# Optimization experiments

Measured on AMD Instinct MI355X. Metric: run time of the kernel, lower is better.

The kernel has to match this reference:

```python
import jax, jax.numpy as jnp
import numpy as np

NUM_HEADS = 16
EPS = 1e-5
CHUNK = 128  # chunk length for the chunked recurrent-state scan


def _linear_attention(x, Wq, Wk, Wv, Wo, bo):
    B, T, E = x.shape
    H = NUM_HEADS
    d = E // H

    def proj(W):
        # nn.Linear(bias=False): y = x @ W.T ; split heads -> (B,H,T,d)
        return (x @ W.T).reshape(B, T, H, d).transpose(0, 2, 1, 3)

    phi_q = jax.nn.elu(proj(Wq)) + 1.0
    phi_k = jax.nn.elu(proj(Wk)) + 1.0
    V = proj(Wv)

    nC = T // CHUNK
    # (nC, B, H, C, d) so lax.scan iterates over chunks of time
    def to_chunks(a):
        return a.reshape(B, H, nC, CHUNK, d).transpose(2, 0, 1, 3, 4)

    qc, kc, vc = to_chunks(phi_q), to_chunks(phi_k), to_chunks(V)
    mask = jnp.tril(jnp.ones((CHUNK, CHUNK), x.dtype))  # causal incl. diagonal

    S0 = jnp.zeros((B, H, d, d), x.dtype)  # running sum of k v^T
    z0 = jnp.zeros((B, H, d), x.dtype)     # running sum of phi_k

    def step(carry, inp):
        S, z = carry
        q, k, v = inp  # (B,H,C,d)
        A = jnp.einsum('bhid,bhjd->bhij', q, k) * mask
        num = jnp.einsum('bhij,bhjd->bhid', A, v) + jnp.einsum('bhid,bhde->bhie', q, S)
        den = jnp.sum(A, axis=-1) + jnp.einsum('bhid,bhd->bhi', q, z) + EPS
        out = num / den[..., None]
        S = S + jnp.einsum('bhjd,bhje->bhde', k, v)
        z = z + jnp.sum(k, axis=2)
        return (S, z), out

    _, outs = jax.lax.scan(step, (S0, z0), (qc, kc, vc))  # (nC,B,H,C,d)
    out = outs.transpose(1, 2, 0, 3, 4).reshape(B, H, T, d)
    out = out.transpose(0, 2, 1, 3).reshape(B, T, E)
    # out_proj (dropout p=0 / eval -> identity)
    return out @ Wo.T + bo


def setup_inputs() -> dict:
    key = jax.random.key(0)
    ks = jax.random.split(key, 6)
    B, T, E = 2, 2048, 1024
    s = 1.0 / np.sqrt(E)
    return {
        'x': jax.random.normal(ks[0], (B, T, E), jnp.float32),
        'Wq': jax.random.normal(ks[1], (E, E), jnp.float32) * s,
        'Wk': jax.random.normal(ks[2], (E, E), jnp.float32) * s,
        'Wv': jax.random.normal(ks[3], (E, E), jnp.float32) * s,
        'Wo': jax.random.normal(ks[4], (E, E), jnp.float32) * s,
        'bo': jnp.zeros((E,), jnp.float32),
    }


def reference(x, Wq, Wk, Wv, Wo, bo):
    return _linear_attention(x, Wq, Wk, Wv, Wo, bo)
```

## Files before the change

kernel.cpp:

```cpp
#include <hip/hip_runtime.h>
#include <hip/hip_bf16.h>
#include <stdint.h>

typedef __attribute__((ext_vector_type(4)))  float  floatx4;
typedef __attribute__((ext_vector_type(8)))  short  short8;
typedef __attribute__((ext_vector_type(8)))  unsigned short ushortx8;
typedef __attribute__((ext_vector_type(4)))  unsigned short ushortx4;

#define B_  2
#define T_  2048
#define E_  1024
#define H_  16
#define D_  64
#define C_  128
#define NC_ 16
#define M_  4096
#define EPS_ 1e-5f

__device__ __forceinline__ unsigned short f2b(float f) {
    union { float f; unsigned int u; } v; v.f = f;
    unsigned int r = v.u + 0x7fffu + ((v.u >> 16) & 1u);
    return (unsigned short)(r >> 16);
}
__device__ __forceinline__ float b2f(unsigned short b) {
    union { unsigned int u; float f; } v; v.u = ((unsigned int)b) << 16;
    return v.f;
}

__device__ __forceinline__ int stage_seg(int i) { return (i & 3) ^ ((i >> 3) & 3); }
__device__ __forceinline__ int frag_slot(int lane) {
    int m = lane & 15, q = lane >> 4;
    return m * 4 + (q ^ ((m >> 1) & 3));
}

__global__ __launch_bounds__(256) void convert_all(const float* __restrict__ x,
                                                   const float* __restrict__ Wq,
                                                   const float* __restrict__ Wk,
                                                   const float* __restrict__ Wv,
                                                   const float* __restrict__ Wo,
                                                   unsigned short* __restrict__ dst) {
    int i = (blockIdx.x * 256 + threadIdx.x) * 4;
    const float* s; int off;
    if (i < M_ * E_) { s = x; off = i; }
    else {
        int j = i - M_ * E_;
        int which = j >> 20;
        s = (which == 0) ? Wq : (which == 1) ? Wk : (which == 2) ? Wv : Wo;
        off = j & ((1 << 20) - 1);
    }
    float4 f = *(const float4*)(s + off);
    ushortx4 o;
    o[0] = f2b(f.x); o[1] = f2b(f.y); o[2] = f2b(f.z); o[3] = f2b(f.w);
    *(ushortx4*)(dst + i) = o;
}

__global__ __launch_bounds__(256) void gemm_qkv(const unsigned short* __restrict__ A,
                                                const unsigned short* __restrict__ Bm,
                                                unsigned short* __restrict__ Cb) {
    const int N = 3 * E_, K = E_;
    __shared__ __align__(16) unsigned short smem[32768];
    unsigned short* at0 = smem;
    unsigned short* bt0 = smem + 8192;
    unsigned short* at1 = smem + 16384;
    unsigned short* bt1 = smem + 24576;
    int tid = threadIdx.x;
    int wave = tid >> 6, lane = tid & 63;
    int wr = wave >> 1, wc = wave & 1;
    int m = lane & 15, q = lane >> 4;
    int srow = lane >> 2, sseg = stage_seg(lane);
    int fs = frag_slot(lane);
    int row0 = blockIdx.y * 128, col0 = blockIdx.x * 128;
    floatx4 acc[4][4];
    for (int i = 0; i < 4; i++) for (int j = 0; j < 4; j++) acc[i][j] = floatx4{0.f, 0.f, 0.f, 0.f};

    auto stageA = [&](unsigned short* at, int k0) {
        for (int p = 0; p < 4; p++) {
            int t = p * 4 + wave;
            const unsigned short* ga = A + (size_t)(row0 + (t & 7) * 16 + srow) * K + k0 + (t >> 3) * 32 + sseg * 8;
            __builtin_amdgcn_global_load_lds((const __attribute__((address_space(1))) unsigned int*)ga,
                (__attribute__((address_space(3))) unsigned int*)(at + t * 512), 16, 0, 0);
        }
    };
    auto stageB = [&](unsigned short* bt, int k0) {
        for (int p = 0; p < 4; p++) {
            int u = p * 4 + wave;
            const unsigned short* gb = Bm + (size_t)(col0 + (u & 7) * 16 + srow) * K + k0 + (u >> 3) * 32 + sseg * 8;
            __builtin_amdgcn_global_load_lds((const __attribute__((address_space(1))) unsigned int*)gb,
                (__attribute__((address_space(3))) unsigned int*)(bt + u * 512), 16, 0, 0);
        }
    };
    short8 af[4], bf[4];
    auto frags = [&](const unsigned short* at, const unsigned short* bt, int kh) {
        for (int mi = 0; mi < 4; mi++) af[mi] = *(const short8*)(at + (kh * 8 + wr * 4 + mi) * 512 + fs * 8);
        for (int ni = 0; ni < 4; ni++) bf[ni] = *(const short8*)(bt + (kh * 8 + wc * 4 + ni) * 512 + fs * 8);
    };
    auto mfma16 = [&]() {
        __builtin_amdgcn_s_setprio(1);
        for (int mi = 0; mi < 4; mi++)
            for (int ni = 0; ni < 4; ni++)
                acc[mi][ni] = __builtin_amdgcn_mfma_f32_16x16x32_bf16(af[mi], bf[ni], acc[mi][ni], 0, 0, 0);
        __builtin_amdgcn_s_setprio(0);
    };

    stageA(at0, 0); stageB(bt0, 0);
    for (int k0 = 0; k0 < K; k0 += 128) {
        stageA(at1, k0 + 64);
        asm volatile("s_waitcnt vmcnt(4)" ::: "memory");
        __builtin_amdgcn_s_barrier();
        frags(at0, bt0, 0);
        mfma16();
        frags(at0, bt0, 1);
        stageB(bt1, k0 + 64);
        mfma16();
        __builtin_amdgcn_s_barrier();
        if (k0 + 128 < K) {
            stageA(at0, k0 + 128);
            asm volatile("s_waitcnt vmcnt(4)" ::: "memory");
        } else {
            asm volatile("s_waitcnt vmcnt(0)" ::: "memory");
        }
        __builtin_amdgcn_s_barrier();
        frags(at1, bt1, 0);
        mfma16();
        frags(at1, bt1, 1);
        if (k0 + 128 < K) stageB(bt0, k0 + 128);
        mfma16();
        __builtin_amdgcn_s_barrier();
    }

    unsigned short* epi = smem + wave * 2176;
    bool isphi = (col0 < 2 * E_);
    for (int half = 0; half < 2; half++) {
        if (half) asm volatile("" ::: "memory");
        for (int mi2 = 0; mi2 < 2; mi2++) {
            int mi = half * 2 + mi2;
            for (int ni = 0; ni < 4; ni++)
                for (int reg = 0; reg < 4; reg++) {
                    int lr = mi2 * 16 + q * 4 + reg;
                    float v = acc[mi][ni][reg];
                    if (isphi) v = (v > 0.f) ? (v + 1.f) : __expf(v);
                    epi[lr * 68 + ni * 16 + m] = f2b(v);
                }
        }
        for (int i = 0; i < 4; i++) {
            int s = i * 64 + lane;
            int lr = s >> 3, seg = s & 7;
            const unsigned short* p = epi + lr * 68 + seg * 8;
            ushortx4 lo = *(const ushortx4*)(p);
            ushortx4 hi = *(const ushortx4*)(p + 4);
            ushortx8 val;
            for (int e = 0; e < 4; e++) { val[e] = lo[e]; val[e + 4] = hi[e]; }
            int row = row0 + wr * 64 + half * 32 + lr;
            int col = col0 + wc * 64 + seg * 8;
            *(ushortx8*)(Cb + (size_t)row * N + col) = val;
        }
    }
}

__global__ __launch_bounds__(256) void gemm_out(const unsigned short* __restrict__ A,
                                                const unsigned short* __restrict__ Bm,
                                                const float* __restrict__ bias,
                                                float* __restrict__ Cf) {
    const int N = E_, K = E_;
    __shared__ __align__(16) unsigned short smem[24576];
    unsigned short* at0 = smem;
    unsigned short* bt0 = smem + 8192;
    unsigned short* at1 = smem + 12288;
    unsigned short* bt1 = smem + 20480;
    int tid = threadIdx.x;
    int wave = tid >> 6, lane = tid & 63;
    int wr = wave >> 1, wc = wave & 1;
    int m = lane & 15, q = lane >> 4;
    int srow = lane >> 2, sseg = stage_seg(lane);
    int fs = frag_slot(lane);
    int row0 = blockIdx.y * 128, col0 = blockIdx.x * 64;
    floatx4 acc[4][2];
    for (int i = 0; i < 4; i++) for (int j = 0; j < 2; j++) acc[i][j] = floatx4{0.f, 0.f, 0.f, 0.f};

    auto stageA = [&](unsigned short* at, int k0) {
        for (int p = 0; p < 4; p++) {
            int t = p * 4 + wave;
            const unsigned short* ga = A + (size_t)(row0 + (t & 7) * 16 + srow) * K + k0 + (t >> 3) * 32 + sseg * 8;
            __builtin_amdgcn_global_load_lds((const __attribute__((address_space(1))) unsigned int*)ga,
                (__attribute__((address_space(3))) unsigned int*)(at + t * 512), 16, 0, 0);
        }
    };
    auto stageB = [&](unsigned short* bt, int k0) {
        for (int p = 0; p < 2; p++) {
            int u = p * 4 + wave;
            const unsigned short* gb = Bm + (size_t)(col0 + (u & 3) * 16 + srow) * K + k0 + (u >> 2) * 32 + sseg * 8;
            __builtin_amdgcn_global_load_lds((const __attribute__((address_space(1))) unsigned int*)gb,
                (__attribute__((address_space(3))) unsigned int*)(bt + u * 512), 16, 0, 0);
        }
    };
    short8 af[4], bf[2];
    auto frags = [&](const unsigned short* at, const unsigned short* bt, int kh) {
        for (int mi = 0; mi < 4; mi++) af[mi] = *(const short8*)(at + (kh * 8 + wr * 4 + mi) * 512 + fs * 8);
        for (int ci = 0; ci < 2; ci++) bf[ci] = *(const short8*)(bt + (kh * 4 + wc * 2 + ci) * 512 + fs * 8);
    };
    auto mfma8 = [&]() {
        __builtin_amdgcn_s_setprio(1);
        for (int mi = 0; mi < 4; mi++)
            for (int ci = 0; ci < 2; ci++)
                acc[mi][ci] = __builtin_amdgcn_mfma_f32_16x16x32_bf16(af[mi], bf[ci], acc[mi][ci], 0, 0, 0);
        __builtin_amdgcn_s_setprio(0);
    };

    stageA(at0, 0); stageB(bt0, 0);
    for (int k0 = 0; k0 < K; k0 += 128) {
        stageA(at1, k0 + 64);
        asm volatile("s_waitcnt vmcnt(4)" ::: "memory");
        __builtin_amdgcn_s_barrier();
        frags(at0, bt0, 0);
        mfma8();
        frags(at0, bt0, 1);
        stageB(bt1, k0 + 64);
        mfma8();
        __builtin_amdgcn_s_barrier();
        if (k0 + 128 < K) {
            stageA(at0, k0 + 128);
            asm volatile("s_waitcnt vmcnt(4)" ::: "memory");
        } else {
            asm volatile("s_waitcnt vmcnt(0)" ::: "memory");
        }
        __builtin_amdgcn_s_barrier();
        frags(at1, bt1, 0);
        mfma8();
        frags(at1, bt1, 1);
        if (k0 + 128 < K) stageB(bt0, k0 + 128);
        mfma8();
        __builtin_amdgcn_s_barrier();
    }

    int qrow = q * 4;
    for (int ci = 0; ci < 2; ci++) {
        int col = col0 + wc * 32 + ci * 16 + m;
        float bv = bias[col];
        for (int mi = 0; mi < 4; mi++)
            for (int r2 = 0; r2 < 4; r2++) {
                int row = row0 + wr * 64 + mi * 16 + qrow + r2;
                Cf[(size_t)row * N + col] = acc[mi][ci][r2] + bv;
            }
    }
}

__global__ __launch_bounds__(256) void chunk_sums(const unsigned short* __restrict__ qkv,
                                                  float* __restrict__ Sc, float* __restrict__ zc) {
    int c = blockIdx.x, h = blockIdx.y, bb = blockIdx.z;
    __shared__ __align__(16) unsigned short Kt[64 * 132];
    __shared__ __align__(16) unsigned short Vt[80 * 132];
    int tid = threadIdx.x;
    int lane = tid & 63, w = tid >> 6;
    size_t rowb = (size_t)bb * T_ + (size_t)c * C_;
    int kcol = E_ + h * D_, vcol = 2 * E_ + h * D_;

    {
        int r4 = (tid >> 3) * 4;
        int seg = (tid & 7) * 8;
        ushortx8 kv[4], vv[4];
        for (int t = 0; t < 4; t++) {
            size_t g = (rowb + r4 + t) * 3072;
            kv[t] = *(const ushortx8*)(qkv + g + kcol + seg);
            vv[t] = *(const ushortx8*)(qkv + g + vcol + seg);
        }
        for (int e = 0; e < 8; e++) {
            ushortx4 ka, va;
            for (int t = 0; t < 4; t++) { ka[t] = kv[t][e]; va[t] = vv[t][e]; }
            *(ushortx4*)(Kt + (seg + e) * 132 + r4) = ka;
            *(ushortx4*)(Vt + (seg + e) * 132 + r4) = va;
        }
    }
    if (tid < 128) Vt[64 * 132 + tid] = 0x3f80;
    __syncthreads();

    floatx4 acc[5];
    for (int ni = 0; ni < 5; ni++) acc[ni] = floatx4{0.f, 0.f, 0.f, 0.f};
    int lm = lane & 15, lk = (lane >> 4) * 8;
    for (int k0 = 0; k0 < 128; k0 += 32) {
        short8 af = *(const short8*)(Kt + (w * 16 + lm) * 132 + k0 + lk);
        for (int ni = 0; ni < 5; ni++) {
            short8 bf = *(const short8*)(Vt + (ni * 16 + lm) * 132 + k0 + lk);
            acc[ni] = __builtin_amdgcn_mfma_f32_16x16x32_bf16(af, bf, acc[ni], 0, 0, 0);
        }
    }
    size_t base = ((size_t)(bb * H_ + h) * NC_ + c) * (size_t)(D_ * D_);
    int r0 = w * 16 + (lane >> 4) * 4;
    for (int ni = 0; ni < 4; ni++)
        for (int reg = 0; reg < 4; reg++)
            Sc[base + (size_t)(r0 + reg) * D_ + ni * 16 + lm] = acc[ni][reg];
    if (lm == 0) {
        size_t zb = ((size_t)(bb * H_ + h) * NC_ + c) * D_;
        for (int reg = 0; reg < 4; reg++) zc[zb + r0 + reg] = acc[4][reg];
    }
}

__global__ __launch_bounds__(256) void prefix_state(const float* __restrict__ Sc,
                                                    const float* __restrict__ zc,
                                                    unsigned short* __restrict__ Spt,
                                                    float* __restrict__ zp) {
    int h = blockIdx.x, bb = blockIdx.y;
    int tid = threadIdx.x;
    size_t bh = (size_t)bb * H_ + h;
    const float* S = Sc + bh * NC_ * (size_t)(D_ * D_);
    unsigned short* P = Spt + bh * NC_ * (size_t)(D_ * D_);
    int p = tid * 16, r = p >> 6, c0 = p & 63;
    float a[16];
    for (int i = 0; i < 16; i++) a[i] = 0.f;
    for (int cc = 0; cc < NC_; cc++) {
        unsigned short* Pc = P + (size_t)cc * (D_ * D_);
        for (int i = 0; i < 16; i++)
            Pc[(c0 + i) * D_ + r] = f2b(a[i]);
        const float* Sj = S + (size_t)cc * (D_ * D_) + p;
        for (int q = 0; q < 16; q += 4) {
            float4 f = *(const float4*)(Sj + q);
            a[q] += f.x; a[q + 1] += f.y; a[q + 2] += f.z; a[q + 3] += f.w;
        }
    }
    if (tid < 64) {
        const float* z = zc + bh * NC_ * (size_t)D_;
        float* zo = zp + bh * NC_ * (size_t)D_;
        float za = 0.f;
        for (int cc = 0; cc < NC_; cc++) { zo[cc * D_ + tid] = za; za += z[cc * D_ + tid]; }
    }
}

__global__ __launch_bounds__(256) void attn_kernel(const unsigned short* __restrict__ qkv,
                                                   const unsigned short* __restrict__ Spt,
                                                   const float* __restrict__ zp,
                                                   unsigned short* __restrict__ attn) {
    int c = blockIdx.x, h = blockIdx.y, bb = blockIdx.z;
    __shared__ __align__(16) unsigned short ks[128 * 68];
    __shared__ __align__(16) unsigned short vt[64 * 132];
    __shared__ __align__(16) unsigned short ovl[128 * 36];
    int tid = threadIdx.x;
    int lane = tid & 63, w = tid >> 6;
    int lm = lane & 15, lq = lane >> 4;
    size_t rowb = (size_t)bb * T_ + (size_t)c * C_;
    int qcol = h * D_, kcol = E_ + h * D_, vcol = 2 * E_ + h * D_;
    size_t pbase = ((size_t)bb * H_ + h) * NC_ + c;

    for (int s = 0; s < 4; s++) {
        int off = s * 256 + tid;
        int r = off >> 3, seg = (off & 7) * 8;
        ushortx8 k8 = *(const ushortx8*)(qkv + (rowb + r) * 3072 + kcol + seg);
        *(ushortx8*)(ks + r * 68 + seg) = k8;
    }
    {
        int r4 = (tid >> 3) * 4;
        int seg = (tid & 7) * 8;
        ushortx8 vv[4];
        for (int t = 0; t < 4; t++)
            vv[t] = *(const ushortx8*)(qkv + (rowb + r4 + t) * 3072 + vcol + seg);
        for (int e = 0; e < 8; e++) {
            ushortx4 va;
            for (int t = 0; t < 4; t++) va[t] = vv[t][e];
            *(ushortx4*)(vt + (seg + e) * 132 + r4) = va;
        }
    }

    short8 aq[2][2];
    for (int mi = 0; mi < 2; mi++)
        for (int kk = 0; kk < 2; kk++)
            aq[mi][kk] = *(const short8*)(qkv + (rowb + w * 32 + mi * 16 + lm) * 3072 + qcol + kk * 32 + lq * 8);

    floatx4 acc[2][4];
    for (int mi = 0; mi < 2; mi++) for (int ni = 0; ni < 4; ni++) acc[mi][ni] = floatx4{0.f, 0.f, 0.f, 0.f};
    {
        const unsigned short* sp = Spt + pbase * (size_t)(D_ * D_);
        for (int kk = 0; kk < 2; kk++)
            for (int ni = 0; ni < 4; ni++) {
                short8 bs = *(const short8*)(sp + (ni * 16 + lm) * D_ + kk * 32 + lq * 8);
                for (int mi = 0; mi < 2; mi++)
                    acc[mi][ni] = __builtin_amdgcn_mfma_f32_16x16x32_bf16(aq[mi][kk], bs, acc[mi][ni], 0, 0, 0);
            }
    }
    float dsum[2][4];
    {
        float4 z4 = *(const float4*)(zp + pbase * D_ + lm * 4);
        for (int mi = 0; mi < 2; mi++)
            for (int reg = 0; reg < 4; reg++) {
                int row = w * 32 + mi * 16 + lq * 4 + reg;
                ushortx4 q4 = *(const ushortx4*)(qkv + (rowb + row) * 3072 + qcol + lm * 4);
                dsum[mi][reg] = b2f(q4[0]) * z4.x + b2f(q4[1]) * z4.y + b2f(q4[2]) * z4.z + b2f(q4[3]) * z4.w;
            }
    }
    __syncthreads();

    for (int jt = 0; jt <= w; jt++) {
        floatx4 pa[2][2];
        for (int mi = 0; mi < 2; mi++) for (int ct = 0; ct < 2; ct++) pa[mi][ct] = floatx4{0.f, 0.f, 0.f, 0.f};
        for (int kk = 0; kk < 2; kk++)
            for (int ct = 0; ct < 2; ct++) {
                short8 bk = *(const short8*)(ks + (jt * 32 + ct * 16 + lm) * 68 + kk * 32 + lq * 8);
                for (int mi = 0; mi < 2; mi++)
                    pa[mi][ct] = __builtin_amdgcn_mfma_f32_16x16x32_bf16(aq[mi][kk], bk, pa[mi][ct], 0, 0, 0);
            }
        bool diag = (jt == w);
        for (int mi = 0; mi < 2; mi++)
            for (int ct = 0; ct < 2; ct++)
                for (int reg = 0; reg < 4; reg++) {
                    int il = mi * 16 + lq * 4 + reg;
                    int jl = ct * 16 + lm;
                    float v = pa[mi][ct][reg];
                    if (diag && jl > il) v = 0.f;
                    dsum[mi][reg] += v;
                    ovl[(w * 32 + il) * 36 + jl] = f2b(v);
                }
        short8 ap[2];
        for (int mi = 0; mi < 2; mi++)
            ap[mi] = *(const short8*)(ovl + (w * 32 + mi * 16 + lm) * 36 + lq * 8);
        for (int ni = 0; ni < 4; ni++) {
            short8 bv = *(const short8*)(vt + (ni * 16 + lm) * 132 + jt * 32 + lq * 8);
            for (int mi = 0; mi < 2; mi++)
                acc[mi][ni] = __builtin_amdgcn_mfma_f32_16x16x32_bf16(ap[mi], bv, acc[mi][ni], 0, 0, 0);
        }
    }

    for (int off = 1; off < 16; off <<= 1)
        for (int mi = 0; mi < 2; mi++)
            for (int reg = 0; reg < 4; reg++)
                dsum[mi][reg] += __shfl_xor(dsum[mi][reg], off);

    for (int mi = 0; mi < 2; mi++)
        for (int reg = 0; reg < 4; reg++) {
            float inv = 1.f / (dsum[mi][reg] + EPS_);
            int row = w * 32 + mi * 16 + lq * 4 + reg;
            for (int ni = 0; ni < 4; ni++)
                attn[(rowb + row) * E_ + h * D_ + ni * 16 + lm] = f2b(acc[mi][ni][reg] * inv);
        }
}

extern "C" void kernel_launch(void* const* d_in, const int* in_sizes, int n_in,
                              void* d_out, int out_size, void* d_ws, size_t ws_size,
                              hipStream_t stream) {
    const float* x  = (const float*)d_in[0];
    const float* Wq = (const float*)d_in[1];
    const float* Wk = (const float*)d_in[2];
    const float* Wv = (const float*)d_in[3];
    const float* Wo = (const float*)d_in[4];
    const float* bo = (const float*)d_in[5];
    float* out = (float*)d_out;

    const size_t MB = 1024 * 1024;
    uint8_t* ws = (uint8_t*)d_ws;
    unsigned short* xb    = (unsigned short*)(ws + 0);
    unsigned short* wb    = (unsigned short*)(ws + 8 * MB);
    unsigned short* wob   = wb + 3 * E_ * E_;
    unsigned short* qkvb  = (unsigned short*)(ws + 16 * MB);
    float* Sc = (float*)(ws + 40 * MB);
    float* zc = (float*)(ws + 48 * MB);
    unsigned short* attnb = xb;
    unsigned short* sptb  = wb;
    float* zpb            = (float*)(ws + 12 * MB);

    convert_all<<<(M_ * E_ + 4 * E_ * E_) / 1024, 256, 0, stream>>>(x, Wq, Wk, Wv, Wo, xb);

    gemm_qkv<<<dim3(24, 32), 256, 0, stream>>>(xb, wb, qkvb);
    chunk_sums<<<dim3(NC_, H_, B_), 256, 0, stream>>>(qkvb, Sc, zc);
    prefix_state<<<dim3(H_, B_), 256, 0, stream>>>(Sc, zc, sptb, zpb);
    attn_kernel<<<dim3(NC_, H_, B_), 256, 0, stream>>>(qkvb, sptb, zpb, attnb);
    gemm_out<<<dim3(16, 32), 256, 0, stream>>>(attnb, wob, bo, out);
}
```

Measured before the change: 164.2 us.

## Widen QKV GEMM tiles to 128x192 and fuse prefix scan into chunk_sums

The QKV projection GEMM now uses 128x192 output tiles: each wave computes a 4x6 block of MFMA fragments, the LDS buffers are enlarged, and the epilogue applies the phi activation per column because a tile can straddle the K/V boundary. The grid shrinks from 768 to 512 blocks, so each block reuses its A tile across more columns. Separately, the prefix_state kernel is removed. Its work now runs in the last chunk_sums block per (batch, head), which is found with an atomic counter that convert_all zeroes. This saves one launch, but it adds more register pressure in the GEMM and leaves the serial prefix scan to a single block per head.

```diff
diff --git a/kernel.cpp b/kernel.cpp
--- a/kernel.cpp
+++ b/kernel.cpp
@@ -38,7 +38,9 @@
                                                    const float* __restrict__ Wk,
                                                    const float* __restrict__ Wv,
                                                    const float* __restrict__ Wo,
-                                                   unsigned short* __restrict__ dst) {
+                                                   unsigned short* __restrict__ dst,
+                                                   unsigned int* __restrict__ cnt) {
+    if (blockIdx.x == 0 && threadIdx.x < 32) cnt[threadIdx.x] = 0;
     int i = (blockIdx.x * 256 + threadIdx.x) * 4;
     const float* s; int off;
     if (i < M_ * E_) { s = x; off = i; }
@@ -58,20 +60,20 @@
                                                 const unsigned short* __restrict__ Bm,
                                                 unsigned short* __restrict__ Cb) {
     const int N = 3 * E_, K = E_;
-    __shared__ __align__(16) unsigned short smem[32768];
+    __shared__ __align__(16) unsigned short smem[40960];
     unsigned short* at0 = smem;
     unsigned short* bt0 = smem + 8192;
-    unsigned short* at1 = smem + 16384;
-    unsigned short* bt1 = smem + 24576;
+    unsigned short* at1 = smem + 20480;
+    unsigned short* bt1 = smem + 28672;
     int tid = threadIdx.x;
     int wave = tid >> 6, lane = tid & 63;
     int wr = wave >> 1, wc = wave & 1;
     int m = lane & 15, q = lane >> 4;
     int srow = lane >> 2, sseg = stage_seg(lane);
     int fs = frag_slot(lane);
-    int row0 = blockIdx.y * 128, col0 = blockIdx.x * 128;
-    floatx4 acc[4][4];
-    for (int i = 0; i < 4; i++) for (int j = 0; j < 4; j++) acc[i][j] = floatx4{0.f, 0.f, 0.f, 0.f};
+    int row0 = blockIdx.y * 128, col0 = blockIdx.x * 192;
+    floatx4 acc[4][6];
+    for (int i = 0; i < 4; i++) for (int j = 0; j < 6; j++) acc[i][j] = floatx4{0.f, 0.f, 0.f, 0.f};
 
     auto stageA = [&](unsigned short* at, int k0) {
         for (int p = 0; p < 4; p++) {
@@ -82,22 +84,23 @@
         }
     };
     auto stageB = [&](unsigned short* bt, int k0) {
-        for (int p = 0; p < 4; p++) {
+        for (int p = 0; p < 6; p++) {
             int u = p * 4 + wave;
-            const unsigned short* gb = Bm + (size_t)(col0 + (u & 7) * 16 + srow) * K + k0 + (u >> 3) * 32 + sseg * 8;
+            int kh = u / 12, rb = u - kh * 12;
+            const unsigned short* gb = Bm + (size_t)(col0 + rb * 16 + srow) * K + k0 + kh * 32 + sseg * 8;
             __builtin_amdgcn_global_load_lds((const __attribute__((address_space(1))) unsigned int*)gb,
                 (__attribute__((address_space(3))) unsigned int*)(bt + u * 512), 16, 0, 0);
         }
     };
-    short8 af[4], bf[4];
+    short8 af[4], bf[6];
     auto frags = [&](const unsigned short* at, const unsigned short* bt, int kh) {
         for (int mi = 0; mi < 4; mi++) af[mi] = *(const short8*)(at + (kh * 8 + wr * 4 + mi) * 512 + fs * 8);
-        for (int ni = 0; ni < 4; ni++) bf[ni] = *(const short8*)(bt + (kh * 8 + wc * 4 + ni) * 512 + fs * 8);
-    };
-    auto mfma16 = [&]() {
+        for (int ni = 0; ni < 6; ni++) bf[ni] = *(const short8*)(bt + (kh * 12 + wc * 6 + ni) * 512 + fs * 8);
+    };
+    auto mfma24 = [&]() {
         __builtin_amdgcn_s_setprio(1);
         for (int mi = 0; mi < 4; mi++)
-            for (int ni = 0; ni < 4; ni++)
+            for (int ni = 0; ni < 6; ni++)
                 acc[mi][ni] = __builtin_amdgcn_mfma_f32_16x16x32_bf16(af[mi], bf[ni], acc[mi][ni], 0, 0, 0);
         __builtin_amdgcn_s_setprio(0);
     };
@@ -108,10 +111,10 @@
         asm volatile("s_waitcnt vmcnt(4)" ::: "memory");
         __builtin_amdgcn_s_barrier();
         frags(at0, bt0, 0);
-        mfma16();
+        mfma24();
         frags(at0, bt0, 1);
         stageB(bt1, k0 + 64);
-        mfma16();
+        mfma24();
         __builtin_amdgcn_s_barrier();
         if (k0 + 128 < K) {
             stageA(at0, k0 + 128);
@@ -121,15 +124,14 @@
         }
         __builtin_amdgcn_s_barrier();
         frags(at1, bt1, 0);
-        mfma16();
+        mfma24();
         frags(at1, bt1, 1);
         if (k0 + 128 < K) stageB(bt0, k0 + 128);
-        mfma16();
+        mfma24();
         __builtin_amdgcn_s_barrier();
     }
 
     unsigned short* epi = smem + wave * 2176;
-    bool isphi = (col0 < 2 * E_);
     for (int half = 0; half < 2; half++) {
         if (half) asm volatile("" ::: "memory");
         for (int mi2 = 0; mi2 < 2; mi2++) {
@@ -137,8 +139,9 @@
             for (int ni = 0; ni < 4; ni++)
                 for (int reg = 0; reg < 4; reg++) {
                     int lr = mi2 * 16 + q * 4 + reg;
+                    int colw = col0 + wc * 96 + ni * 16 + m;
                     float v = acc[mi][ni][reg];
-                    if (isphi) v = (v > 0.f) ? (v + 1.f) : __expf(v);
+                    if (colw < 2 * E_) v = (v > 0.f) ? (v + 1.f) : __expf(v);
                     epi[lr * 68 + ni * 16 + m] = f2b(v);
                 }
         }
@@ -151,7 +154,32 @@
             ushortx8 val;
             for (int e = 0; e < 4; e++) { val[e] = lo[e]; val[e + 4] = hi[e]; }
             int row = row0 + wr * 64 + half * 32 + lr;
-            int col = col0 + wc * 64 + seg * 8;
+            int col = col0 + wc * 96 + seg * 8;
+            *(ushortx8*)(Cb + (size_t)row * N + col) = val;
+        }
+        asm volatile("" ::: "memory");
+        for (int mi2 = 0; mi2 < 2; mi2++) {
+            int mi = half * 2 + mi2;
+            for (int ni = 4; ni < 6; ni++)
+                for (int reg = 0; reg < 4; reg++) {
+                    int lr = mi2 * 16 + q * 4 + reg;
+                    int colw = col0 + wc * 96 + ni * 16 + m;
+                    float v = acc[mi][ni][reg];
+                    if (colw < 2 * E_) v = (v > 0.f) ? (v + 1.f) : __expf(v);
+                    epi[lr * 36 + (ni - 4) * 16 + m] = f2b(v);
+                }
+        }
+        asm volatile("" ::: "memory");
+        for (int i = 0; i < 2; i++) {
+            int s = i * 64 + lane;
+            int lr = s >> 2, seg = s & 3;
+            const unsigned short* p = epi + lr * 36 + seg * 8;
+            ushortx4 lo = *(const ushortx4*)(p);
+            ushortx4 hi = *(const ushortx4*)(p + 4);
+            ushortx8 val;
+            for (int e = 0; e < 4; e++) { val[e] = lo[e]; val[e + 4] = hi[e]; }
+            int row = row0 + wr * 64 + half * 32 + lr;
+            int col = col0 + wc * 96 + 64 + seg * 8;
             *(ushortx8*)(Cb + (size_t)row * N + col) = val;
         }
     }
@@ -245,14 +273,19 @@
 }
 
 __global__ __launch_bounds__(256) void chunk_sums(const unsigned short* __restrict__ qkv,
-                                                  float* __restrict__ Sc, float* __restrict__ zc) {
+                                                  float* __restrict__ Sc, float* __restrict__ zc,
+                                                  unsigned short* __restrict__ Spt,
+                                                  float* __restrict__ zp,
+                                                  unsigned int* __restrict__ cnt) {
     int c = blockIdx.x, h = blockIdx.y, bb = blockIdx.z;
     __shared__ __align__(16) unsigned short Kt[64 * 132];
     __shared__ __align__(16) unsigned short Vt[80 * 132];
+    __shared__ unsigned int lastflag;
     int tid = threadIdx.x;
     int lane = tid & 63, w = tid >> 6;
     size_t rowb = (size_t)bb * T_ + (size_t)c * C_;
     int kcol = E_ + h * D_, vcol = 2 * E_ + h * D_;
+    size_t bh = (size_t)bb * H_ + h;
 
     {
         int r4 = (tid >> 3) * 4;
@@ -283,24 +316,22 @@
             acc[ni] = __builtin_amdgcn_mfma_f32_16x16x32_bf16(af, bf, acc[ni], 0, 0, 0);
         }
     }
-    size_t base = ((size_t)(bb * H_ + h) * NC_ + c) * (size_t)(D_ * D_);
+    size_t base = (bh * NC_ + c) * (size_t)(D_ * D_);
     int r0 = w * 16 + (lane >> 4) * 4;
     for (int ni = 0; ni < 4; ni++)
         for (int reg = 0; reg < 4; reg++)
             Sc[base + (size_t)(r0 + reg) * D_ + ni * 16 + lm] = acc[ni][reg];
     if (lm == 0) {
-        size_t zb = ((size_t)(bb * H_ + h) * NC_ + c) * D_;
+        size_t zb = (bh * NC_ + c) * D_;
         for (int reg = 0; reg < 4; reg++) zc[zb + r0 + reg] = acc[4][reg];
     }
-}
-
-__global__ __launch_bounds__(256) void prefix_state(const float* __restrict__ Sc,
-                                                    const float* __restrict__ zc,
-                                                    unsigned short* __restrict__ Spt,
-                                                    float* __restrict__ zp) {
-    int h = blockIdx.x, bb = blockIdx.y;
-    int tid = threadIdx.x;
-    size_t bh = (size_t)bb * H_ + h;
+
+    __threadfence();
+    if (tid == 0) lastflag = (atomicAdd(&cnt[bh], 1u) == NC_ - 1u);
+    __syncthreads();
+    if (!lastflag) return;
+    __threadfence();
+
     const float* S = Sc + bh * NC_ * (size_t)(D_ * D_);
     unsigned short* P = Spt + bh * NC_ * (size_t)(D_ * D_);
     int p = tid * 16, r = p >> 6, c0 = p & 63;
@@ -311,9 +342,9 @@
         for (int i = 0; i < 16; i++)
             Pc[(c0 + i) * D_ + r] = f2b(a[i]);
         const float* Sj = S + (size_t)cc * (D_ * D_) + p;
-        for (int q = 0; q < 16; q += 4) {
-            float4 f = *(const float4*)(Sj + q);
-            a[q] += f.x; a[q + 1] += f.y; a[q + 2] += f.z; a[q + 3] += f.w;
+        for (int qq = 0; qq < 16; qq += 4) {
+            float4 f = *(const float4*)(Sj + qq);
+            a[qq] += f.x; a[qq + 1] += f.y; a[qq + 2] += f.z; a[qq + 3] += f.w;
         }
     }
     if (tid < 64) {
@@ -452,12 +483,12 @@
     unsigned short* attnb = xb;
     unsigned short* sptb  = wb;
     float* zpb            = (float*)(ws + 12 * MB);
-
-    convert_all<<<(M_ * E_ + 4 * E_ * E_) / 1024, 256, 0, stream>>>(x, Wq, Wk, Wv, Wo, xb);
-
-    gemm_qkv<<<dim3(24, 32), 256, 0, stream>>>(xb, wb, qkvb);
-    chunk_sums<<<dim3(NC_, H_, B_), 256, 0, stream>>>(qkvb, Sc, zc);
-    prefix_state<<<dim3(H_, B_), 256, 0, stream>>>(Sc, zc, sptb, zpb);
+    unsigned int* cntb    = (unsigned int*)(ws + 49 * MB);
+
+    convert_all<<<(M_ * E_ + 4 * E_ * E_) / 1024, 256, 0, stream>>>(x, Wq, Wk, Wv, Wo, xb, cntb);
+
+    gemm_qkv<<<dim3(16, 32), 256, 0, stream>>>(xb, wb, qkvb);
+    chunk_sums<<<dim3(NC_, H_, B_), 256, 0, stream>>>(qkvb, Sc, zc, sptb, zpb, cntb);
     attn_kernel<<<dim3(NC_, H_, B_), 256, 0, stream>>>(qkvb, sptb, zpb, attnb);
     gemm_out<<<dim3(16, 32), 256, 0, stream>>>(attnb, wob, bo, out);
 }
```

Measured after the change: 246.0 us. +49.8%, slower.
